# Kernel optimization log

Measured on AMD Instinct MI355X. Metric: run time of the kernel, lower is better.

## Reference

```python
import jax, jax.numpy as jnp
from jax import lax
import numpy as np
import math

B, T, D, H, DFF, L = 64, 351, 512, 8, 1024, 3
DK = D // H
SQRT_DIM = math.sqrt(D)


def setup_inputs() -> dict:
    key = jax.random.key(0)
    ks = jax.random.split(key, 32)
    s = 0.02
    n = lambda k, shape, sc=s: jax.random.normal(k, shape, jnp.float32) * sc
    inp = {
        'x': jax.random.normal(ks[0], (B, T, D), jnp.float32),
        'mask': jax.random.normal(ks[1], (B, T, D), jnp.float32),  # float stream: used as pos_embedding inside attention
        'pos_emb': n(ks[2], (L, T, D)),           # Encoder.pos_embedding_{1,2,3}
        'Wq': n(ks[3], (L, D, D)), 'bq': jnp.zeros((L, D), jnp.float32),
        'Wk': n(ks[4], (L, D, D)), 'bk': jnp.zeros((L, D), jnp.float32),
        'Wv': n(ks[5], (L, D, D)), 'bv': jnp.zeros((L, D), jnp.float32),
        'Wp': n(ks[6], (L, D, D)),                 # pos_proj, no bias
        'u_bias': n(ks[7], (L, H, DK)), 'v_bias': n(ks[8], (L, H, DK)),
        'Wo': n(ks[9], (L, D, D)), 'bo': jnp.zeros((L, D), jnp.float32),
        'ln1_a': jnp.ones((L, D), jnp.float32), 'ln1_b': jnp.zeros((L, D), jnp.float32),
        'ln2_a': jnp.ones((L, D), jnp.float32), 'ln2_b': jnp.zeros((L, D), jnp.float32),
        'W1': n(ks[10], (L, DFF, D)), 'b1': jnp.zeros((L, DFF), jnp.float32),   # conv1d k=1
        'W2': n(ks[11], (L, D, DFF, 3)), 'b2': jnp.zeros((L, D), jnp.float32),  # conv1d k=3 pad=1
        'fn_a': jnp.ones((D,), jnp.float32), 'fn_b': jnp.zeros((D,), jnp.float32),
    }
    return inp


def layernorm(x, a, b, eps=1e-6):
    # torch: a*(x-mean)/(std+eps)+b with unbiased std (Bessel, n-1)
    mean = x.mean(-1, keepdims=True)
    xc = x - mean
    std = jnp.sqrt((xc * xc).sum(-1, keepdims=True) / (x.shape[-1] - 1))
    return a * xc / (std + eps) + b


def rel_shift(ps):
    # Transformer-XL relative shift via pad+reshape
    b, h, t1, t2 = ps.shape
    p = jnp.pad(ps, ((0, 0), (0, 0), (0, 0), (1, 0)))
    p = p.reshape(b, h, t2 + 1, t1)
    return p[:, :, 1:].reshape(b, h, t1, t2)


def attention(xn, pe, Wq, bq, Wk, bk, Wv, bv, Wp, u, v, Wo, bo):
    b, t, _ = xn.shape
    q = (xn @ Wq.T + bq).reshape(b, t, H, DK)
    k = (xn @ Wk.T + bk).reshape(b, t, H, DK)
    val = (xn @ Wv.T + bv).reshape(b, t, H, DK)
    p = (pe @ Wp.T).reshape(b, t, H, DK)
    content = jnp.einsum('bqhd,bkhd->bhqk', q + u, k)
    pos = rel_shift(jnp.einsum('bqhd,bkhd->bhqk', q + v, p))
    attn = jax.nn.softmax((content + pos) / SQRT_DIM, axis=-1)  # mask=None path; dropout inactive (eval)
    ctx = jnp.einsum('bhqk,bkhd->bqhd', attn, val).reshape(b, t, D)
    return ctx @ Wo.T + bo


def reference(x, mask, pos_emb, Wq, bq, Wk, bk, Wv, bv, Wp, u_bias, v_bias, Wo, bo,
              ln1_a, ln1_b, ln2_a, ln2_b, W1, b1, W2, b2, fn_a, fn_b):
    for i in range(L):
        x = x + pos_emb[i][None]
        # sublayer 0: pre-LN relative MHA with residual (stride_num[i]==1)
        xn = layernorm(x, ln1_a[i], ln1_b[i])
        x = x + attention(xn, mask, Wq[i], bq[i], Wk[i], bk[i], Wv[i], bv[i],
                          Wp[i], u_bias[i], v_bias[i], Wo[i], bo[i])
        # sublayer 1: pre-LN conv FFN (k=1 conv -> ReLU -> k=3 conv, pad 1, stride 1)
        xn = layernorm(x, ln2_a[i], ln2_b[i])
        h = jax.nn.relu(jnp.einsum('btd,fd->btf', xn, W1[i]) + b1[i])
        y = lax.conv_general_dilated(h.transpose(0, 2, 1), W2[i], (1,), [(1, 1)],
                                     dimension_numbers=('NCH', 'OIH', 'NCH'))
        x = x + (y + b2[i][None, :, None]).transpose(0, 2, 1)
    return layernorm(x, fn_a, fn_b)
```

## Files before the change

kernel.cpp:

```cpp
#include <hip/hip_runtime.h>
#include <hip/hip_bf16.h>

typedef __hip_bfloat16 bf16;
typedef __attribute__((ext_vector_type(8))) short short8;
typedef __attribute__((ext_vector_type(4))) float f32x4;

constexpr int BB  = 64;
constexpr int TT  = 351;
constexpr int DD  = 512;
constexpr int HH  = 8;
constexpr int DK  = 64;
constexpr int FF  = 1024;
constexpr int LL  = 3;
constexpr int MT  = BB * TT;
constexpr int TD  = TT * DD;

constexpr int QT  = 32;
constexpr int NQT = (TT + QT - 1) / QT;

constexpr size_t LW      = 3407872;
constexpr size_t OFF_QKV = 0;
constexpr size_t OFF_P   = 786432;
constexpr size_t OFF_O   = 1048576;
constexpr size_t OFF_W1  = 1310720;
constexpr size_t OFF_W2  = 1835008;

__device__ __forceinline__ float us2f(unsigned short u) {
    union { unsigned int i; float f; } c; c.i = ((unsigned int)u) << 16; return c.f;
}
__device__ __forceinline__ float bf2f(bf16 h) { return __bfloat162float(h); }
__device__ __forceinline__ bf16  f2bf(float f) { return __float2bfloat16(f); }
__device__ __forceinline__ float ldin(const void* p, size_t i, bool f32) {
    return f32 ? ((const float*)p)[i] : bf2f(((const bf16*)p)[i]);
}
__device__ __forceinline__ unsigned short f2us(float f) {
    bf16 h = f2bf(f); return *reinterpret_cast<unsigned short*>(&h);
}

__global__ void detect_kernel(const unsigned short* ln1a, int* flag) {
    if (threadIdx.x == 0 && blockIdx.x == 0)
        *flag = (ln1a[0] == 0) ? 1 : 0;
}

__global__ __launch_bounds__(256) void cvt_kernel(
    const void* __restrict__ src, size_t S, size_t slstride,
    bf16* __restrict__ dst, size_t doff, int nl, int mode,
    const int* __restrict__ dflag)
{
    const bool f32 = (*dflag != 0);
    size_t i = (size_t)blockIdx.x * 256 + threadIdx.x;
    size_t total = (size_t)nl * S;
    if (i >= total) return;
    size_t l = i / S, e = i - l * S;
    size_t se;
    if (mode == 1) {
        size_t j = e >> 19;
        size_t nf = e & ((1u << 19) - 1);
        size_t n = nf >> 10, f = nf & 1023;
        se = n * 3072 + f * 3 + j;
    } else se = e;
    dst[doff + l * LW + e] = f2bf(ldin(src, l * slstride + se, f32));
}

__global__ __launch_bounds__(256) void addpos_kernel(
    const void* __restrict__ xin, const void* __restrict__ pos, size_t posoff,
    float* __restrict__ xf, int init, const int* __restrict__ dflag)
{
    const bool f32 = (*dflag != 0);
    int i = blockIdx.x * 256 + threadIdx.x;
    if (i >= MT * DD) return;
    int td = i % TD;
    float p = ldin(pos, posoff + td, f32);
    if (init) xf[i] = ldin(xin, i, f32) + p;
    else      xf[i] += p;
}

__global__ __launch_bounds__(256) void ln_kernel(
    const float* __restrict__ xf, const void* __restrict__ ga, size_t gaoff,
    const void* __restrict__ gb, size_t gboff,
    void* __restrict__ out, int final_o, const int* __restrict__ dflag)
{
    const bool f32 = (*dflag != 0);
    __shared__ float red[256];
    const int row = blockIdx.x;
    const int tid = threadIdx.x;
    const float* xr = xf + (size_t)row * DD;
    float x0 = xr[tid], x1 = xr[tid + 256];

    red[tid] = x0 + x1;
    __syncthreads();
    for (int o = 128; o > 0; o >>= 1) {
        if (tid < o) red[tid] += red[tid + o];
        __syncthreads();
    }
    float mean = red[0] * (1.0f / 512.0f);
    __syncthreads();
    float c0 = x0 - mean, c1 = x1 - mean;
    red[tid] = c0 * c0 + c1 * c1;
    __syncthreads();
    for (int o = 128; o > 0; o >>= 1) {
        if (tid < o) red[tid] += red[tid + o];
        __syncthreads();
    }
    float stdv = sqrtf(red[0] * (1.0f / 511.0f));
    float inv = 1.0f / (stdv + 1e-6f);
    float v0 = ldin(ga, gaoff + tid,       f32) * c0 * inv + ldin(gb, gboff + tid,       f32);
    float v1 = ldin(ga, gaoff + tid + 256, f32) * c1 * inv + ldin(gb, gboff + tid + 256, f32);
    if (final_o && f32) {
        float* orow = (float*)out + (size_t)row * DD;
        orow[tid] = v0; orow[tid + 256] = v1;
    } else {
        bf16* orow = (bf16*)out + (size_t)row * DD;
        orow[tid] = f2bf(v0); orow[tid + 256] = f2bf(v1);
    }
}

__global__ __launch_bounds__(256) void mgemm_kernel(
    const void* __restrict__ A, size_t aoff, int a_ext,
    const bf16* __restrict__ W,
    const void* __restrict__ b0, const void* __restrict__ b1p,
    const void* __restrict__ b2p, size_t boff,
    void* __restrict__ outp, int M, int N, int K, int mode, int chN,
    const int* __restrict__ dflag)
{
    const bool f32 = (*dflag != 0);
    const bool a32 = a_ext && f32;
    __shared__ unsigned short As[128][40];
    __shared__ unsigned short Bs[128][40];
    const int tid = threadIdx.x;
    const int n0 = blockIdx.x * 128, m0 = blockIdx.y * 128;

    const int lane = tid & 63, wv = tid >> 6;
    const int wm = wv >> 1, wn = wv & 1;
    const int q = lane >> 4, lm = lane & 15;

    f32x4 acc[4][4] = {};

    for (int k0 = 0; k0 < K; k0 += 32) {
        #pragma unroll
        for (int part = 0; part < 2; ++part) {
            int idx = part * 256 + tid;
            int row = idx >> 2;
            int seg = (idx & 3) * 8;
            int grow = m0 + row; if (grow >= M) grow = M - 1;
            if (a32) {
                const float* ap = (const float*)A + aoff + (size_t)grow * K + k0 + seg;
                union { unsigned short us[8]; int4 v; } t;
                #pragma unroll
                for (int e = 0; e < 8; ++e) t.us[e] = f2us(ap[e]);
                *(int4*)&As[row][seg] = t.v;
            } else {
                *(int4*)&As[row][seg] =
                    *(const int4*)((const bf16*)A + aoff + (size_t)grow * K + k0 + seg);
            }
            *(int4*)&Bs[row][seg] =
                *(const int4*)(W + (size_t)(n0 + row) * K + k0 + seg);
        }
        __syncthreads();
        short8 af[4], bfv[4];
        #pragma unroll
        for (int i = 0; i < 4; ++i) af[i]  = *(const short8*)&As[wm * 64 + i * 16 + lm][q * 8];
        #pragma unroll
        for (int j = 0; j < 4; ++j) bfv[j] = *(const short8*)&Bs[wn * 64 + j * 16 + lm][q * 8];
        #pragma unroll
        for (int i = 0; i < 4; ++i)
            #pragma unroll
            for (int j = 0; j < 4; ++j)
                acc[i][j] = __builtin_amdgcn_mfma_f32_16x16x32_bf16(af[i], bfv[j], acc[i][j], 0, 0, 0);
        __syncthreads();
    }

    #pragma unroll
    for (int i = 0; i < 4; ++i) {
        #pragma unroll
        for (int j = 0; j < 4; ++j) {
            #pragma unroll
            for (int r = 0; r < 4; ++r) {
                int m = m0 + wm * 64 + i * 16 + q * 4 + r;
                if (m >= M) continue;
                int n = n0 + wn * 64 + j * 16 + lm;
                float c = acc[i][j][r];
                if (mode == 0) {
                    int which = n >> 9;
                    int nn = n & 511;
                    const void* bp = which == 0 ? b0 : (which == 1 ? b1p : b2p);
                    if (bp) c += ldin(bp, boff + nn, f32);
                    int b = m / TT, t = m - b * TT;
                    int h = nn >> 6, dk = nn & 63;
                    ((bf16*)outp)[(size_t)which * chN +
                                  ((((size_t)b * HH + h) * TT + t) * DK) + dk] = f2bf(c);
                } else if (mode == 1) {
                    if (b0) c += ldin(b0, boff + n, f32);
                    ((bf16*)outp)[(size_t)m * N + n] = f2bf(fmaxf(c, 0.0f));
                } else {
                    if (b0) c += ldin(b0, boff + n, f32);
                    ((float*)outp)[(size_t)m * DD + n] += c;
                }
            }
        }
    }
}

__global__ __launch_bounds__(256) void mconv_kernel(
    const bf16* __restrict__ Hb, const bf16* __restrict__ Wc,
    const void* __restrict__ bias, size_t boff,
    float* __restrict__ xf, int M, const int* __restrict__ dflag)
{
    const bool f32 = (*dflag != 0);
    __shared__ unsigned short As[128][40];
    __shared__ unsigned short Bs[128][40];
    const int tid = threadIdx.x;
    const int n0 = blockIdx.x * 128, m0 = blockIdx.y * 128;

    const int lane = tid & 63, wv = tid >> 6;
    const int wm = wv >> 1, wn = wv & 1;
    const int q = lane >> 4, lm = lane & 15;

    int rowP[2], segP[2], mloadP[2], trowP[2];
    bool inrP[2];
    #pragma unroll
    for (int part = 0; part < 2; ++part) {
        int idx = part * 256 + tid;
        rowP[part] = idx >> 2;
        segP[part] = (idx & 3) * 8;
        int mrow = m0 + rowP[part];
        inrP[part] = mrow < M;
        int mload = inrP[part] ? mrow : (M - 1);
        mloadP[part] = mload;
        trowP[part] = mload % TT;
    }

    f32x4 acc[4][4] = {};

    for (int j = 0; j < 3; ++j) {
        for (int k0 = 0; k0 < FF; k0 += 32) {
            #pragma unroll
            for (int part = 0; part < 2; ++part) {
                int row = rowP[part], seg = segP[part];
                int ts = trowP[part] + j - 1;
                bool valid = inrP[part] && ts >= 0 && ts < TT;
                if (valid) {
                    *(int4*)&As[row][seg] =
                        *(const int4*)(Hb + (size_t)(mloadP[part] + j - 1) * FF + k0 + seg);
                } else {
                    int4 z = {0, 0, 0, 0};
                    *(int4*)&As[row][seg] = z;
                }
                *(int4*)&Bs[row][seg] =
                    *(const int4*)(Wc + (size_t)j * 524288 + (size_t)(n0 + row) * FF + k0 + seg);
            }
            __syncthreads();
            short8 af[4], bfv[4];
            #pragma unroll
            for (int i = 0; i < 4; ++i) af[i]  = *(const short8*)&As[wm * 64 + i * 16 + lm][q * 8];
            #pragma unroll
            for (int jj = 0; jj < 4; ++jj) bfv[jj] = *(const short8*)&Bs[wn * 64 + jj * 16 + lm][q * 8];
            #pragma unroll
            for (int i = 0; i < 4; ++i)
                #pragma unroll
                for (int jj = 0; jj < 4; ++jj)
                    acc[i][jj] = __builtin_amdgcn_mfma_f32_16x16x32_bf16(af[i], bfv[jj], acc[i][jj], 0, 0, 0);
            __syncthreads();
        }
    }

    #pragma unroll
    for (int i = 0; i < 4; ++i) {
        #pragma unroll
        for (int jj = 0; jj < 4; ++jj) {
            #pragma unroll
            for (int r = 0; r < 4; ++r) {
                int m = m0 + wm * 64 + i * 16 + q * 4 + r;
                if (m >= M) continue;
                int n = n0 + wn * 64 + jj * 16 + lm;
                xf[(size_t)m * DD + n] += acc[i][jj][r] + ldin(bias, boff + n, f32);
            }
        }
    }
}

__global__ __launch_bounds__(256) void attn_kernel(
    const bf16* __restrict__ Q, const bf16* __restrict__ Kb,
    const bf16* __restrict__ V, const bf16* __restrict__ P,
    const void* __restrict__ ubias, const void* __restrict__ vbias, size_t uvoff,
    bf16* __restrict__ ctx, const int* __restrict__ dflag)
{
    const bool f32 = (*dflag != 0);
    const int qt = blockIdx.x;
    const int h  = blockIdx.y;
    const int b  = blockIdx.z;
    const int q0 = qt * QT;
    const int tid  = threadIdx.x;
    const int lane = tid & 63;
    const int wv   = tid >> 6;
    const int lm   = lane & 15;
    const int q8   = lane >> 4;

    __shared__ __align__(16) char sbuf[46080];
    float (*S)[356] = reinterpret_cast<float(*)[356]>(sbuf);
    unsigned short (*Vt)[360] = reinterpret_cast<unsigned short(*)[360]>(sbuf);

    __shared__ __align__(16) unsigned short Abf[QT][360];
    __shared__ __align__(16) unsigned short qu[32][72];
    __shared__ __align__(16) unsigned short qv[48][72];

    const size_t base = (((size_t)b * HH + h) * TT) * DK;
    const float scale = 0.04419417382415922f;

    for (int i = tid; i < 48 * 64; i += 256) {
        int q = i >> 6, d = i & 63;
        int qrow = q0 + q;
        float qq = (qrow < TT) ? bf2f(Q[base + (size_t)qrow * DK + d]) : 0.0f;
        float vb = ldin(vbias, uvoff + h * DK + d, f32);
        qv[q][d] = (qrow < TT) ? f2us((qq + vb) * scale) : (unsigned short)0;
        if (q < 32) {
            float ub = ldin(ubias, uvoff + h * DK + d, f32);
            qu[q][d] = f2us((qq + ub) * scale);
        }
    }
    __syncthreads();

    {
        short8 af0a = *(const short8*)&qu[lm][q8 * 8];
        short8 af0b = *(const short8*)&qu[lm][32 + q8 * 8];
        short8 af1a = *(const short8*)&qu[16 + lm][q8 * 8];
        short8 af1b = *(const short8*)&qu[16 + lm][32 + q8 * 8];
        for (int jt = wv; jt < 22; jt += 4) {
            int kr = jt * 16 + lm; if (kr > TT - 1) kr = TT - 1;
            const short8* kp = (const short8*)(Kb + base + (size_t)kr * DK + q8 * 8);
            short8 bv0 = kp[0];
            short8 bv1 = kp[4];
            f32x4 a0 = {}, a1 = {};
            a0 = __builtin_amdgcn_mfma_f32_16x16x32_bf16(af0a, bv0, a0, 0, 0, 0);
            a0 = __builtin_amdgcn_mfma_f32_16x16x32_bf16(af0b, bv1, a0, 0, 0, 0);
            a1 = __builtin_amdgcn_mfma_f32_16x16x32_bf16(af1a, bv0, a1, 0, 0, 0);
            a1 = __builtin_amdgcn_mfma_f32_16x16x32_bf16(af1b, bv1, a1, 0, 0, 0);
            int col = jt * 16 + lm;
            #pragma unroll
            for (int r = 0; r < 4; ++r) {
                S[q8 * 4 + r][col]      = a0[r];
                S[16 + q8 * 4 + r][col] = a1[r];
            }
        }
    }
    __syncthreads();

    {
        short8 af[3][2];
        #pragma unroll
        for (int i = 0; i < 3; ++i) {
            af[i][0] = *(const short8*)&qv[i * 16 + lm][q8 * 8];
            af[i][1] = *(const short8*)&qv[i * 16 + lm][32 + q8 * 8];
        }
        for (int jt = wv; jt < 22; jt += 4) {
            int pr = jt * 16 + lm; if (pr > TT - 1) pr = TT - 1;
            const short8* pp = (const short8*)(P + base + (size_t)pr * DK + q8 * 8);
            short8 bv0 = pp[0];
            short8 bv1 = pp[4];
            f32x4 acc[3] = {};
            #pragma unroll
            for (int i = 0; i < 3; ++i) {
                acc[i] = __builtin_amdgcn_mfma_f32_16x16x32_bf16(af[i][0], bv0, acc[i], 0, 0, 0);
                acc[i] = __builtin_amdgcn_mfma_f32_16x16x32_bf16(af[i][1], bv1, acc[i], 0, 0, 0);
            }
            int j = jt * 16 + lm;
            if (j < TT) {
                #pragma unroll
                for (int i = 0; i < 3; ++i) {
                    #pragma unroll
                    for (int r = 0; r < 4; ++r) {
                        int rl = i * 16 + q8 * 4 + r;
                        int rg = q0 + rl;
                        float v = acc[i][r];
                        if (j >= TT - 1 - rg) {
                            if (rl < QT) S[rl][j - (TT - 1) + rg] += v;
                        } else {
                            if (rl >= 1 && rl <= QT) S[rl - 1][j + rg + 1] += v;
                        }
                    }
                }
            }
        }
    }
    __syncthreads();

    {
        const int row = tid >> 3, k0 = tid & 7;
        float* Sr = S[row];
        float m = -1e30f;
        for (int k = k0; k < TT; k += 8) m = fmaxf(m, Sr[k]);
        #pragma unroll
        for (int msk = 1; msk < 8; msk <<= 1) m = fmaxf(m, __shfl_xor(m, msk));
        float sum = 0.0f;
        for (int k = k0; k < TT; k += 8) {
            float e = __expf(Sr[k] - m);
            Sr[k] = e;
            sum += e;
        }
        #pragma unroll
        for (int msk = 1; msk < 8; msk <<= 1) sum += __shfl_xor(sum, msk);
        float rinv = 1.0f / sum;
        for (int k = k0; k < 360; k += 8)
            Abf[row][k] = (k < TT) ? f2us(Sr[k] * rinv) : (unsigned short)0;
    }
    __syncthreads();

    for (int idx = tid; idx < 176 * 8; idx += 256) {
        int p2 = idx >> 3, dsg = idx & 7;
        int k0r = p2 * 2;
        const short8 v0 = *(const short8*)(V + base + (size_t)k0r * DK + dsg * 8);
        int k1 = (k0r + 1 < TT) ? (k0r + 1) : k0r;
        const short8 v1 = *(const short8*)(V + base + (size_t)k1 * DK + dsg * 8);
        const bool hasv1 = (k0r + 1 < TT);
        #pragma unroll
        for (int e = 0; e < 8; ++e) {
            unsigned int pk = (unsigned int)(unsigned short)v0[e];
            if (hasv1) pk |= ((unsigned int)(unsigned short)v1[e]) << 16;
            *(unsigned int*)&Vt[dsg * 8 + e][k0r] = pk;
        }
    }
    __syncthreads();

    {
        f32x4 a0 = {}, a1 = {};
        for (int ks = 0; ks < 11; ++ks) {
            short8 bv  = *(const short8*)&Vt[wv * 16 + lm][ks * 32 + q8 * 8];
            short8 av0 = *(const short8*)&Abf[lm][ks * 32 + q8 * 8];
            short8 av1 = *(const short8*)&Abf[16 + lm][ks * 32 + q8 * 8];
            a0 = __builtin_amdgcn_mfma_f32_16x16x32_bf16(av0, bv, a0, 0, 0, 0);
            a1 = __builtin_amdgcn_mfma_f32_16x16x32_bf16(av1, bv, a1, 0, 0, 0);
        }
        const int d = wv * 16 + lm;
        #pragma unroll
        for (int r = 0; r < 4; ++r) {
            int qrow = q0 + q8 * 4 + r;
            if (qrow < TT)
                ctx[((size_t)b * TT + qrow) * DD + h * DK + d] = f2bf(a0[r]);
            qrow = q0 + 16 + q8 * 4 + r;
            if (qrow < TT)
                ctx[((size_t)b * TT + qrow) * DD + h * DK + d] = f2bf(a1[r]);
        }
    }
}

extern "C" void kernel_launch(void* const* d_in, const int* in_sizes, int n_in,
                              void* d_out, int out_size, void* d_ws, size_t ws_size,
                              hipStream_t stream)
{
    (void)in_sizes; (void)n_in; (void)out_size;
    const void* x    = d_in[0];
    const void* mask = d_in[1];
    const void* pos  = d_in[2];
    const void* Wq   = d_in[3];
    const void* bq   = d_in[4];
    const void* Wk   = d_in[5];
    const void* bk   = d_in[6];
    const void* Wv   = d_in[7];
    const void* bv   = d_in[8];
    const void* Wp   = d_in[9];
    const void* ub   = d_in[10];
    const void* vbi  = d_in[11];
    const void* Wo   = d_in[12];
    const void* bo   = d_in[13];
    const void* l1a  = d_in[14];
    const void* l1b  = d_in[15];
    const void* l2a  = d_in[16];
    const void* l2b  = d_in[17];
    const void* W1   = d_in[18];
    const void* b1   = d_in[19];
    const void* W2   = d_in[20];
    const void* b2   = d_in[21];
    const void* fa   = d_in[22];
    const void* fb   = d_in[23];

    const size_t exf = (size_t)MT * DD;
    char* w = (char*)d_ws;
    int*   dflag = (int*)w;
    float* xf = (float*)(w + 256);
    bf16*  xn = (bf16*)(w + 256 + exf * 4);
    bf16*  sc = (bf16*)(w + 256 + exf * 6);
    bf16*  wbuf = (bf16*)d_out;

    const size_t fixed = 256 + exf * 6;
    int cha = 8;
    if      (ws_size >= fixed + (size_t)4 * 64 * TT * DD * 2) cha = 64;
    else if (ws_size >= fixed + (size_t)4 * 32 * TT * DD * 2) cha = 32;
    else if (ws_size >= fixed + (size_t)4 * 16 * TT * DD * 2) cha = 16;
    const int nca = BB / cha;
    const int ma  = cha * TT;
    const int chf = (cha * 2 > 64) ? 64 : cha * 2;
    const int ncf = BB / chf;
    const int mf  = chf * TT;
    const int chN = ma * DD;

    bf16* qc = sc;
    bf16* pc = sc + (size_t)3 * chN;
    bf16* hb = sc;

    dim3 blk(256);
    dim3 g_ep((MT * DD + 255) / 256);
    dim3 g_ln(MT);
    dim3 g_qkv(12, (ma + 127) / 128);
    dim3 g_p(4, (ma + 127) / 128);
    dim3 g_attn(NQT, HH, cha);
    dim3 g_o(4, (MT + 127) / 128);
    dim3 g_f1(8, (mf + 127) / 128);
    dim3 g_cv(4, (mf + 127) / 128);

    detect_kernel<<<dim3(1), dim3(64), 0, stream>>>((const unsigned short*)l1a, dflag);

    auto cvt = [&](const void* src, size_t S, size_t doff, int mode) {
        dim3 g((unsigned)(((size_t)3 * S + 255) / 256));
        cvt_kernel<<<g, blk, 0, stream>>>(src, S, S, wbuf, doff, 3, mode, dflag);
    };
    cvt(Wq, 262144, OFF_QKV,          0);
    cvt(Wk, 262144, OFF_QKV + 262144, 0);
    cvt(Wv, 262144, OFF_QKV + 524288, 0);
    cvt(Wp, 262144, OFF_P,            0);
    cvt(Wo, 262144, OFF_O,            0);
    cvt(W1, 524288, OFF_W1,           0);
    cvt(W2, 1572864, OFF_W2,          1);

    for (int l = 0; l < LL; ++l) {
        const bf16* wl = wbuf + (size_t)l * LW;
        addpos_kernel<<<g_ep, blk, 0, stream>>>(x, pos, (size_t)l * TD, xf, l == 0, dflag);
        ln_kernel<<<g_ln, blk, 0, stream>>>(xf, l1a, (size_t)l * DD, l1b, (size_t)l * DD, xn, 0, dflag);
        for (int c = 0; c < nca; ++c) {
            bf16* xnc = xn + (size_t)c * ma * DD;
            mgemm_kernel<<<g_qkv, blk, 0, stream>>>(xnc, 0, 0, wl + OFF_QKV,
                bq, bk, bv, (size_t)l * DD, qc, ma, 1536, DD, 0, chN, dflag);
            mgemm_kernel<<<g_p, blk, 0, stream>>>(mask, (size_t)c * ma * DD, 1, wl + OFF_P,
                nullptr, nullptr, nullptr, 0, pc, ma, DD, DD, 0, 0, dflag);
            attn_kernel<<<g_attn, blk, 0, stream>>>(qc, qc + chN, qc + 2 * (size_t)chN, pc,
                ub, vbi, (size_t)l * HH * DK, xnc, dflag);
        }
        mgemm_kernel<<<g_o, blk, 0, stream>>>(xn, 0, 0, wl + OFF_O,
            bo, nullptr, nullptr, (size_t)l * DD, xf, MT, DD, DD, 2, 0, dflag);
        ln_kernel<<<g_ln, blk, 0, stream>>>(xf, l2a, (size_t)l * DD, l2b, (size_t)l * DD, xn, 0, dflag);
        for (int c = 0; c < ncf; ++c) {
            mgemm_kernel<<<g_f1, blk, 0, stream>>>(xn + (size_t)c * mf * DD, 0, 0, wl + OFF_W1,
                b1, nullptr, nullptr, (size_t)l * FF, hb, mf, FF, DD, 1, 0, dflag);
            mconv_kernel<<<g_cv, blk, 0, stream>>>(hb, wl + OFF_W2,
                b2, (size_t)l * DD, xf + (size_t)c * mf * DD, mf, dflag);
        }
    }
    ln_kernel<<<g_ln, blk, 0, stream>>>(xf, fa, 0, fb, 0, d_out, 1, dflag);
}
```

Before: 2.782 ms.

## Prefetch K/P/V tiles into registers and remap attention block order for L2 reuse

```diff
diff --git a/kernel.cpp b/kernel.cpp
--- a/kernel.cpp
+++ b/kernel.cpp
@@ -286,10 +286,14 @@
     bf16* __restrict__ ctx, const int* __restrict__ dflag)
 {
     const bool f32 = (*dflag != 0);
-    const int qt = blockIdx.x;
-    const int h  = blockIdx.y;
-    const int b  = blockIdx.z;
-    const int q0 = qt * QT;
+    const int d  = blockIdx.x + NQT * (blockIdx.y + HH * blockIdx.z);
+    const int rr = d % (8 * NQT);
+    const int g  = (d / (8 * NQT)) * 8 + (rr & 7);
+    const int t  = rr >> 3;
+    const int b  = g >> 3;
+    const int h  = g & 7;
+    const int q0 = t * QT;
+
     const int tid  = threadIdx.x;
     const int lane = tid & 63;
     const int wv   = tid >> 6;
@@ -308,33 +312,43 @@
     const float scale = 0.04419417382415922f;
 
     for (int i = tid; i < 48 * 64; i += 256) {
-        int q = i >> 6, d = i & 63;
+        int q = i >> 6, dd = i & 63;
         int qrow = q0 + q;
-        float qq = (qrow < TT) ? bf2f(Q[base + (size_t)qrow * DK + d]) : 0.0f;
-        float vb = ldin(vbias, uvoff + h * DK + d, f32);
-        qv[q][d] = (qrow < TT) ? f2us((qq + vb) * scale) : (unsigned short)0;
+        float qq = (qrow < TT) ? bf2f(Q[base + (size_t)qrow * DK + dd]) : 0.0f;
+        float vb = ldin(vbias, uvoff + h * DK + dd, f32);
+        qv[q][dd] = (qrow < TT) ? f2us((qq + vb) * scale) : (unsigned short)0;
         if (q < 32) {
-            float ub = ldin(ubias, uvoff + h * DK + d, f32);
-            qu[q][d] = f2us((qq + ub) * scale);
-        }
-    }
-    __syncthreads();
+            float ub = ldin(ubias, uvoff + h * DK + dd, f32);
+            qu[q][dd] = f2us((qq + ub) * scale);
+        }
+    }
+    __syncthreads();
+
+    short8 kv0[6], kv1[6], pv0[6], pv1[6];
+    #pragma unroll
+    for (int it = 0; it < 6; ++it) {
+        int jt = wv + it * 4;
+        int kr = jt * 16 + lm; if (kr > TT - 1) kr = TT - 1;
+        const short8* kp = (const short8*)(Kb + base + (size_t)kr * DK + q8 * 8);
+        const short8* pp = (const short8*)(P  + base + (size_t)kr * DK + q8 * 8);
+        kv0[it] = kp[0]; kv1[it] = kp[4];
+        pv0[it] = pp[0]; pv1[it] = pp[4];
+    }
 
     {
         short8 af0a = *(const short8*)&qu[lm][q8 * 8];
         short8 af0b = *(const short8*)&qu[lm][32 + q8 * 8];
         short8 af1a = *(const short8*)&qu[16 + lm][q8 * 8];
         short8 af1b = *(const short8*)&qu[16 + lm][32 + q8 * 8];
-        for (int jt = wv; jt < 22; jt += 4) {
-            int kr = jt * 16 + lm; if (kr > TT - 1) kr = TT - 1;
-            const short8* kp = (const short8*)(Kb + base + (size_t)kr * DK + q8 * 8);
-            short8 bv0 = kp[0];
-            short8 bv1 = kp[4];
+        #pragma unroll
+        for (int it = 0; it < 6; ++it) {
+            int jt = wv + it * 4;
+            if (jt >= 22) break;
             f32x4 a0 = {}, a1 = {};
-            a0 = __builtin_amdgcn_mfma_f32_16x16x32_bf16(af0a, bv0, a0, 0, 0, 0);
-            a0 = __builtin_amdgcn_mfma_f32_16x16x32_bf16(af0b, bv1, a0, 0, 0, 0);
-            a1 = __builtin_amdgcn_mfma_f32_16x16x32_bf16(af1a, bv0, a1, 0, 0, 0);
-            a1 = __builtin_amdgcn_mfma_f32_16x16x32_bf16(af1b, bv1, a1, 0, 0, 0);
+            a0 = __builtin_amdgcn_mfma_f32_16x16x32_bf16(af0a, kv0[it], a0, 0, 0, 0);
+            a0 = __builtin_amdgcn_mfma_f32_16x16x32_bf16(af0b, kv1[it], a0, 0, 0, 0);
+            a1 = __builtin_amdgcn_mfma_f32_16x16x32_bf16(af1a, kv0[it], a1, 0, 0, 0);
+            a1 = __builtin_amdgcn_mfma_f32_16x16x32_bf16(af1b, kv1[it], a1, 0, 0, 0);
             int col = jt * 16 + lm;
             #pragma unroll
             for (int r = 0; r < 4; ++r) {
@@ -352,16 +366,15 @@
             af[i][0] = *(const short8*)&qv[i * 16 + lm][q8 * 8];
             af[i][1] = *(const short8*)&qv[i * 16 + lm][32 + q8 * 8];
         }
-        for (int jt = wv; jt < 22; jt += 4) {
-            int pr = jt * 16 + lm; if (pr > TT - 1) pr = TT - 1;
-            const short8* pp = (const short8*)(P + base + (size_t)pr * DK + q8 * 8);
-            short8 bv0 = pp[0];
-            short8 bv1 = pp[4];
+        #pragma unroll
+        for (int it = 0; it < 6; ++it) {
+            int jt = wv + it * 4;
+            if (jt >= 22) break;
             f32x4 acc[3] = {};
             #pragma unroll
             for (int i = 0; i < 3; ++i) {
-                acc[i] = __builtin_amdgcn_mfma_f32_16x16x32_bf16(af[i][0], bv0, acc[i], 0, 0, 0);
-                acc[i] = __builtin_amdgcn_mfma_f32_16x16x32_bf16(af[i][1], bv1, acc[i], 0, 0, 0);
+                acc[i] = __builtin_amdgcn_mfma_f32_16x16x32_bf16(af[i][0], pv0[it], acc[i], 0, 0, 0);
+                acc[i] = __builtin_amdgcn_mfma_f32_16x16x32_bf16(af[i][1], pv1[it], acc[i], 0, 0, 0);
             }
             int j = jt * 16 + lm;
             if (j < TT) {
@@ -371,12 +384,10 @@
                     for (int r = 0; r < 4; ++r) {
                         int rl = i * 16 + q8 * 4 + r;
                         int rg = q0 + rl;
-                        float v = acc[i][r];
-                        if (j >= TT - 1 - rg) {
-                            if (rl < QT) S[rl][j - (TT - 1) + rg] += v;
-                        } else {
-                            if (rl >= 1 && rl <= QT) S[rl - 1][j + rg + 1] += v;
-                        }
+                        int cb  = (j + rg < TT - 1) ? 1 : 0;
+                        int row = rl - cb;
+                        int col = j + rg - (TT - 1) + cb * TT;
+                        if (row >= 0 && row < QT) S[row][col] += acc[i][r];
                     }
                 }
             }
@@ -405,18 +416,32 @@
     }
     __syncthreads();
 
-    for (int idx = tid; idx < 176 * 8; idx += 256) {
-        int p2 = idx >> 3, dsg = idx & 7;
-        int k0r = p2 * 2;
-        const short8 v0 = *(const short8*)(V + base + (size_t)k0r * DK + dsg * 8);
-        int k1 = (k0r + 1 < TT) ? (k0r + 1) : k0r;
-        const short8 v1 = *(const short8*)(V + base + (size_t)k1 * DK + dsg * 8);
-        const bool hasv1 = (k0r + 1 < TT);
-        #pragma unroll
-        for (int e = 0; e < 8; ++e) {
-            unsigned int pk = (unsigned int)(unsigned short)v0[e];
-            if (hasv1) pk |= ((unsigned int)(unsigned short)v1[e]) << 16;
-            *(unsigned int*)&Vt[dsg * 8 + e][k0r] = pk;
+    {
+        short8 v0[6], v1[6];
+        #pragma unroll
+        for (int it = 0; it < 6; ++it) {
+            int idx = it * 256 + tid;
+            int p2 = idx >> 3, dsg = idx & 7;
+            if (p2 > 175) p2 = 175;
+            int k0r = p2 * 2;
+            v0[it] = *(const short8*)(V + base + (size_t)k0r * DK + dsg * 8);
+            int k1 = (k0r + 1 < TT) ? (k0r + 1) : k0r;
+            v1[it] = *(const short8*)(V + base + (size_t)k1 * DK + dsg * 8);
+        }
+        #pragma unroll
+        for (int it = 0; it < 6; ++it) {
+            int idx = it * 256 + tid;
+            if (idx < 176 * 8) {
+                int p2 = idx >> 3, dsg = idx & 7;
+                int k0r = p2 * 2;
+                const bool hasv1 = (k0r + 1 < TT);
+                #pragma unroll
+                for (int e = 0; e < 8; ++e) {
+                    unsigned int pk = (unsigned int)(unsigned short)v0[it][e];
+                    if (hasv1) pk |= ((unsigned int)(unsigned short)v1[it][e]) << 16;
+                    *(unsigned int*)&Vt[dsg * 8 + e][k0r] = pk;
+                }
+            }
         }
     }
     __syncthreads();
@@ -430,15 +455,15 @@
             a0 = __builtin_amdgcn_mfma_f32_16x16x32_bf16(av0, bv, a0, 0, 0, 0);
             a1 = __builtin_amdgcn_mfma_f32_16x16x32_bf16(av1, bv, a1, 0, 0, 0);
         }
-        const int d = wv * 16 + lm;
+        const int dd = wv * 16 + lm;
         #pragma unroll
         for (int r = 0; r < 4; ++r) {
             int qrow = q0 + q8 * 4 + r;
             if (qrow < TT)
-                ctx[((size_t)b * TT + qrow) * DD + h * DK + d] = f2bf(a0[r]);
+                ctx[((size_t)b * TT + qrow) * DD + h * DK + dd] = f2bf(a0[r]);
             qrow = q0 + 16 + q8 * 4 + r;
             if (qrow < TT)
-                ctx[((size_t)b * TT + qrow) * DD + h * DK + d] = f2bf(a1[r]);
+                ctx[((size_t)b * TT + qrow) * DD + h * DK + dd] = f2bf(a1[r]);
         }
     }
 }
```

After: 2.630 ms. 1.06x faster.
